# Optimization experiments

Hardware: AMD Instinct MI355X
Metric: run time of the kernel (lower is better)

The kernel has to match this reference:

```python
import jax, jax.numpy as jnp
import numpy as np
import math

DIM = 1024
HEADS = 16
DH = DIM // HEADS
HIDDEN = 4 * DIM
B, N = 2, 1024
DT = 0.05


def _cplx(r, i):
    return jax.lax.complex(r, i)


def clin(x, Wr, Wi, br, bi):
    # complex linear: (xr + i xi)(Wr + i Wi)^T + (br + i bi)
    xr, xi = x.real, x.imag
    real = xr @ Wr.T - xi @ Wi.T + br
    imag = xr @ Wi.T + xi @ Wr.T + bi
    return _cplx(real, imag)


def setup_inputs() -> dict:
    key = jax.random.key(0)
    ks = jax.random.split(key, 32)
    s = 0.02
    d = {
        'x_real': jax.random.normal(ks[0], (B, N, DIM), jnp.float32),
        'x_imag': jax.random.normal(ks[1], (B, N, DIM), jnp.float32),
    }
    i = 2
    for name in ['q', 'k', 'v', 'o']:
        d[f'Wr_{name}'] = jax.random.normal(ks[i], (DIM, DIM), jnp.float32) * s; i += 1
        d[f'Wi_{name}'] = jax.random.normal(ks[i], (DIM, DIM), jnp.float32) * s; i += 1
        d[f'br_{name}'] = jnp.zeros((DIM,), jnp.float32)
        d[f'bi_{name}'] = jnp.zeros((DIM,), jnp.float32)
    d['Wr_f1'] = jax.random.normal(ks[i], (HIDDEN, DIM), jnp.float32) * s; i += 1
    d['Wi_f1'] = jax.random.normal(ks[i], (HIDDEN, DIM), jnp.float32) * s; i += 1
    d['br_f1'] = jnp.zeros((HIDDEN,), jnp.float32)
    d['bi_f1'] = jnp.zeros((HIDDEN,), jnp.float32)
    d['Wr_f2'] = jax.random.normal(ks[i], (DIM, HIDDEN), jnp.float32) * s; i += 1
    d['Wi_f2'] = jax.random.normal(ks[i], (DIM, HIDDEN), jnp.float32) * s; i += 1
    d['br_f2'] = jnp.zeros((DIM,), jnp.float32)
    d['bi_f2'] = jnp.zeros((DIM,), jnp.float32)
    H0 = jax.random.normal(ks[i], (DIM, DIM), jnp.float32) * s; i += 1
    d['H'] = (H0 + H0.T) / 2
    d['dt'] = jnp.float32(DT)
    return d


def _forward(x_real, x_imag,
             Wr_q, Wi_q, br_q, bi_q, Wr_k, Wi_k, br_k, bi_k,
             Wr_v, Wi_v, br_v, bi_v, Wr_o, Wi_o, br_o, bi_o,
             Wr_f1, Wi_f1, br_f1, bi_f1, Wr_f2, Wi_f2, br_f2, bi_f2,
             H, dt):
    x = _cplx(x_real, x_imag)  # [B,N,D] complex64
    scale = 1.0 / math.sqrt(DH)

    # --- Quantum Fourier attention ---
    def heads(t):
        return t.reshape(B, N, HEADS, DH).transpose(0, 2, 1, 3)  # [B,H,N,dh]
    Q = heads(clin(x, Wr_q, Wi_q, br_q, bi_q))
    K = heads(clin(x, Wr_k, Wi_k, br_k, bi_k))
    V = heads(clin(x, Wr_v, Wi_v, br_v, bi_v))
    Qf = jnp.fft.fft(Q, axis=2)
    Kf = jnp.fft.fft(K, axis=2)
    Vf = jnp.fft.fft(V, axis=2)
    scores = jnp.einsum('bhid,bhjd->bhij', Qf, jnp.conj(Kf)) * scale
    attn = jax.nn.softmax(scores.real, axis=-1).astype(jnp.complex64)
    out_f = jnp.einsum('bhij,bhjd->bhid', attn, Vf)
    out = jnp.fft.ifft(out_f, axis=2).transpose(0, 2, 1, 3).reshape(B, N, DIM)
    attn_out = clin(out, Wr_o, Wi_o, br_o, bi_o)
    x = x + attn_out

    # --- Quantum feed-forward (GELU on real & imag separately, exact erf) ---
    h = clin(x, Wr_f1, Wi_f1, br_f1, bi_f1)
    h = _cplx(jax.nn.gelu(h.real, approximate=False),
              jax.nn.gelu(h.imag, approximate=False))
    x = x + clin(h, Wr_f2, Wi_f2, br_f2, bi_f2)

    # --- Schrodinger unitary evolution: U = expm(-i H dt) ---
    A = _cplx(jnp.zeros_like(H), -(H * dt))  # complex64
    U = jax.scipy.linalg.expm(A)
    out = (x.reshape(B * N, DIM) @ U).reshape(B, N, DIM)
    return out


def reference(x_real, x_imag,
              Wr_q, Wi_q, br_q, bi_q, Wr_k, Wi_k, br_k, bi_k,
              Wr_v, Wi_v, br_v, bi_v, Wr_o, Wi_o, br_o, bi_o,
              Wr_f1, Wi_f1, br_f1, bi_f1, Wr_f2, Wi_f2, br_f2, bi_f2,
              H, dt):
    out = _forward(x_real, x_imag,
                   Wr_q, Wi_q, br_q, bi_q, Wr_k, Wi_k, br_k, bi_k,
                   Wr_v, Wi_v, br_v, bi_v, Wr_o, Wi_o, br_o, bi_o,
                   Wr_f1, Wi_f1, br_f1, bi_f1, Wr_f2, Wi_f2, br_f2, bi_f2,
                   H, dt)
    # return real/imag stacked for easy real-valued comparison: [2,B,N,D]
    return jnp.stack([out.real, out.imag], axis=0)
```

## Files before the change

### kernel.cpp

```cpp
#include <hip/hip_runtime.h>
#include <cstdint>
#include <cstddef>

typedef unsigned int u32;
typedef unsigned short u16;
typedef long long i64;

typedef __attribute__((ext_vector_type(8))) short short8;
typedef __attribute__((ext_vector_type(4))) float f32x4;
typedef __attribute__((ext_vector_type(4))) int i32x4;

__device__ __forceinline__ u16 f2bf(float f) {
  u32 u = __float_as_uint(f);
  u = (u + 0x7FFFu + ((u >> 16) & 1u)) >> 16;
  return (u16)u;
}
__device__ __forceinline__ float bf2f(u16 h) { return __uint_as_float(((u32)h) << 16); }

__device__ __forceinline__ short8 neg8(short8 v) {
  i32x4 u = __builtin_bit_cast(i32x4, v);
  u = u ^ (int)0x80008000u;
  return __builtin_bit_cast(short8, u);
}
__device__ __forceinline__ f32x4 mfma16(short8 a, short8 b, f32x4 c) {
  return __builtin_amdgcn_mfma_f32_16x16x32_bf16(a, b, c, 0, 0, 0);
}
__device__ __forceinline__ float gelu_f(float x) {
  return 0.5f * x * (1.0f + erff(x * 0.7071067811865475f));
}
__device__ __forceinline__ void gl16(const u16* g, u16* l) {
  __builtin_amdgcn_global_load_lds((const __attribute__((address_space(1))) void*)g,
                                   (__attribute__((address_space(3))) void*)l, 16, 0, 0);
}
template <int N>
__device__ __forceinline__ void wait_barrier() {
  asm volatile("s_waitcnt vmcnt(%0)\n\ts_barrier" ::"i"(N) : "memory");
}

struct GemmP {
  const u16 *Arh, *Aih, *Arl, *Ail;
  const u16 *Brh, *Bih, *Brl, *Bil;
  const float *biasr, *biasi;
  const float *Resr, *Resi;
  float *Cr32, *Ci32;
  u16 *Crh, *Cih, *Crl, *Cil;
  i64 sA1, sA2, sB1, sB2, sC1, sC2;
  int ZH;
  int M, N, K, lda, ldb, ldc;
  float alpha;
  int beta, wb32, ctrans, bias_mode, bias_period, gelu, splitB;
  float bias_scale;
};

template <int CMODE, int SPLIT, int DEEP>
__global__ __launch_bounds__(256, 2) void cgemm_kernel(GemmP p) {
  constexpr bool HAS_CI = (CMODE == 0 || CMODE == 2 || CMODE == 3);
  constexpr bool AI = (CMODE == 0 || CMODE == 3);
  constexpr bool BIc = (CMODE == 0 || CMODE == 2 || CMODE == 3);
  constexpr int BUFU = SPLIT ? 24576 : 8192;
  constexpr int NBUF = DEEP ? 3 : 1;
  __shared__ u16 smem[BUFU * NBUF];
  constexpr int LPS64 = 2 + (AI ? 1 : 0) + (BIc ? 1 : 0);
  constexpr int NJ = SPLIT ? 4 : 2;

  const int tid = threadIdx.x, lane = tid & 63, wave = tid >> 6;
  const int lrow = lane & 15, quad = lane >> 4;
  const int wr = wave >> 1, wc = wave & 1;
  const int m0 = blockIdx.y * (SPLIT ? 128 : 64);
  const int n0 = blockIdx.x * 64;
  const int z1 = blockIdx.z / p.ZH, z2 = blockIdx.z % p.ZH;
  const i64 zA = (i64)z1 * p.sA1 + (i64)z2 * p.sA2;
  const i64 zB = (i64)z1 * p.sB1 + (i64)z2 * p.sB2;
  const i64 zC = (i64)z1 * p.sC1 + (i64)z2 * p.sC2;
  const int l4 = lane >> 2;
  const int lc = DEEP ? ((((lane & 3) ^ ((lane >> 3) & 3))) << 3) : ((lane & 3) << 3);
  const i64 aoff0 = zA + (i64)(m0 + (SPLIT ? 32 : 16) * wave + l4) * p.lda + lc;
  const i64 aoff1 = aoff0 + (i64)16 * p.lda;
  const i64 boff = zB + (i64)(n0 + 16 * wave + l4) * p.ldb + lc;
  const int lA0 = (SPLIT ? 1024 : 512) * wave, lA1 = lA0 + 512;
  const int lB0 = 512 * wave;
  const int cxw = ((lrow >> 1) & 3) << 3;

  f32x4 accR[2][NJ], accI[2][NJ];
  const f32x4 z4 = {0.f, 0.f, 0.f, 0.f};
#pragma unroll
  for (int i = 0; i < 2; ++i)
#pragma unroll
    for (int j = 0; j < NJ; ++j) { accR[i][j] = z4; accI[i][j] = z4; }

  const int ktn = p.K >> 5;

  if constexpr (SPLIT && !DEEP) {
    for (int kt = 0; kt < ktn; ++kt) {
      const i64 kc = (i64)(kt << 5);
      __syncthreads();
      gl16(p.Arh + aoff0 + kc, smem + lA0);
      gl16(p.Arh + aoff1 + kc, smem + lA1);
      gl16(p.Aih + aoff0 + kc, smem + 4096 + lA0);
      gl16(p.Aih + aoff1 + kc, smem + 4096 + lA1);
      gl16(p.Arl + aoff0 + kc, smem + 8192 + lA0);
      gl16(p.Arl + aoff1 + kc, smem + 8192 + lA1);
      gl16(p.Ail + aoff0 + kc, smem + 12288 + lA0);
      gl16(p.Ail + aoff1 + kc, smem + 12288 + lA1);
      gl16(p.Brh + boff + kc, smem + 16384 + lB0);
      gl16(p.Bih + boff + kc, smem + 18432 + lB0);
      if (p.splitB) {
        gl16(p.Brl + boff + kc, smem + 20480 + lB0);
        gl16(p.Bil + boff + kc, smem + 22528 + lB0);
      }
      __syncthreads();

      short8 bRh[4], bIh[4], bRl[4], bIl[4];
#pragma unroll
      for (int j = 0; j < 4; ++j) {
        const int off = (j * 16 + lrow) * 32 + quad * 8;
        bRh[j] = *(const short8*)&smem[16384 + off];
        bIh[j] = *(const short8*)&smem[18432 + off];
        if (p.splitB) {
          bRl[j] = *(const short8*)&smem[20480 + off];
          bIl[j] = *(const short8*)&smem[22528 + off];
        }
      }
#pragma unroll
      for (int i = 0; i < 2; ++i) {
        const int off = (wave * 32 + i * 16 + lrow) * 32 + quad * 8;
        short8 aRh = *(const short8*)&smem[off];
        short8 aIh = *(const short8*)&smem[4096 + off];
        short8 aRl = *(const short8*)&smem[8192 + off];
        short8 aIl = *(const short8*)&smem[12288 + off];
        if constexpr (CMODE == 0) {
          short8 nIh = neg8(aIh), nIl = neg8(aIl);
#pragma unroll
          for (int j = 0; j < 4; ++j) {
            accR[i][j] = mfma16(aRh, bRh[j], accR[i][j]);
            accR[i][j] = mfma16(nIh, bIh[j], accR[i][j]);
            accI[i][j] = mfma16(aRh, bIh[j], accI[i][j]);
            accI[i][j] = mfma16(aIh, bRh[j], accI[i][j]);
            accR[i][j] = mfma16(aRl, bRh[j], accR[i][j]);
            accR[i][j] = mfma16(nIl, bIh[j], accR[i][j]);
            accI[i][j] = mfma16(aRl, bIh[j], accI[i][j]);
            accI[i][j] = mfma16(aIl, bRh[j], accI[i][j]);
            if (p.splitB) {
              accR[i][j] = mfma16(aRh, bRl[j], accR[i][j]);
              accR[i][j] = mfma16(nIh, bIl[j], accR[i][j]);
              accI[i][j] = mfma16(aRh, bIl[j], accI[i][j]);
              accI[i][j] = mfma16(aIh, bRl[j], accI[i][j]);
            }
          }
        } else {
#pragma unroll
          for (int j = 0; j < 4; ++j) {
            accR[i][j] = mfma16(aRh, bRh[j], accR[i][j]);
            accR[i][j] = mfma16(aIh, bIh[j], accR[i][j]);
            accR[i][j] = mfma16(aRl, bRh[j], accR[i][j]);
            accR[i][j] = mfma16(aIl, bIh[j], accR[i][j]);
            accR[i][j] = mfma16(aRh, bRl[j], accR[i][j]);
            accR[i][j] = mfma16(aIh, bIl[j], accR[i][j]);
          }
        }
      }
    }
  } else if constexpr (SPLIT && DEEP) {
    auto stageS = [&](int buf, i64 kc) {
      u16* s = smem + buf * 24576;
      gl16(p.Arh + aoff0 + kc, s + lA0);
      gl16(p.Arh + aoff1 + kc, s + lA1);
      gl16(p.Aih + aoff0 + kc, s + 4096 + lA0);
      gl16(p.Aih + aoff1 + kc, s + 4096 + lA1);
      gl16(p.Arl + aoff0 + kc, s + 8192 + lA0);
      gl16(p.Arl + aoff1 + kc, s + 8192 + lA1);
      gl16(p.Ail + aoff0 + kc, s + 12288 + lA0);
      gl16(p.Ail + aoff1 + kc, s + 12288 + lA1);
      gl16(p.Brh + boff + kc, s + 16384 + lB0);
      gl16(p.Bih + boff + kc, s + 18432 + lB0);
      if (p.splitB) {
        gl16(p.Brl + boff + kc, s + 20480 + lB0);
        gl16(p.Bil + boff + kc, s + 22528 + lB0);
      }
    };
    if (ktn > 0) stageS(0, 0);
    if (ktn > 1) stageS(1, 32);
    for (int kt = 0; kt < ktn; ++kt) {
      if (kt + 1 < ktn) {
        if (p.splitB) wait_barrier<12>(); else wait_barrier<10>();
      } else {
        wait_barrier<0>();
      }
      if (kt + 2 < ktn) stageS((kt + 2) % 3, (i64)((kt + 2) << 5));
      const u16* sb = smem + (kt % 3) * 24576;

      short8 bRh[4], bIh[4], bRl[4], bIl[4];
#pragma unroll
      for (int j = 0; j < 4; ++j) {
        const int off = (j * 16 + lrow) * 32 + (quad * 8 ^ cxw);
        bRh[j] = *(const short8*)&sb[16384 + off];
        bIh[j] = *(const short8*)&sb[18432 + off];
        if (p.splitB) {
          bRl[j] = *(const short8*)&sb[20480 + off];
          bIl[j] = *(const short8*)&sb[22528 + off];
        }
      }
#pragma unroll
      for (int i = 0; i < 2; ++i) {
        const int off = (wave * 32 + i * 16 + lrow) * 32 + (quad * 8 ^ cxw);
        short8 aRh = *(const short8*)&sb[off];
        short8 aIh = *(const short8*)&sb[4096 + off];
        short8 aRl = *(const short8*)&sb[8192 + off];
        short8 aIl = *(const short8*)&sb[12288 + off];
        if constexpr (CMODE == 0) {
          short8 nIh = neg8(aIh), nIl = neg8(aIl);
#pragma unroll
          for (int j = 0; j < 4; ++j) {
            accR[i][j] = mfma16(aRh, bRh[j], accR[i][j]);
            accR[i][j] = mfma16(nIh, bIh[j], accR[i][j]);
            accI[i][j] = mfma16(aRh, bIh[j], accI[i][j]);
            accI[i][j] = mfma16(aIh, bRh[j], accI[i][j]);
            accR[i][j] = mfma16(aRl, bRh[j], accR[i][j]);
            accR[i][j] = mfma16(nIl, bIh[j], accR[i][j]);
            accI[i][j] = mfma16(aRl, bIh[j], accI[i][j]);
            accI[i][j] = mfma16(aIl, bRh[j], accI[i][j]);
            if (p.splitB) {
              accR[i][j] = mfma16(aRh, bRl[j], accR[i][j]);
              accR[i][j] = mfma16(nIh, bIl[j], accR[i][j]);
              accI[i][j] = mfma16(aRh, bIl[j], accI[i][j]);
              accI[i][j] = mfma16(aIh, bRl[j], accI[i][j]);
            }
          }
        } else {
#pragma unroll
          for (int j = 0; j < 4; ++j) {
            accR[i][j] = mfma16(aRh, bRh[j], accR[i][j]);
            accR[i][j] = mfma16(aIh, bIh[j], accR[i][j]);
            accR[i][j] = mfma16(aRl, bRh[j], accR[i][j]);
            accR[i][j] = mfma16(aIl, bIh[j], accR[i][j]);
            accR[i][j] = mfma16(aRh, bRl[j], accR[i][j]);
            accR[i][j] = mfma16(aIh, bIl[j], accR[i][j]);
          }
        }
      }
    }
  } else {
    auto stage = [&](int buf, i64 kc) {
      u16* s = smem + buf * 8192;
      gl16(p.Arh + aoff0 + kc, s + lA0);
      if constexpr (AI) gl16(p.Aih + aoff0 + kc, s + 2048 + lA0);
      gl16(p.Brh + boff + kc, s + 4096 + lB0);
      if constexpr (BIc) gl16(p.Bih + boff + kc, s + 6144 + lB0);
    };
    if (ktn > 0) stage(0, 0);
    if (ktn > 1) stage(1, 32);
    for (int kt = 0; kt < ktn; ++kt) {
      if (kt + 1 < ktn) wait_barrier<LPS64>(); else wait_barrier<0>();
      if (kt + 2 < ktn) stage((kt + 2) % 3, (i64)((kt + 2) << 5));
      const u16* sb = smem + (kt % 3) * 8192;

      short8 bR[2], bI[2];
#pragma unroll
      for (int j = 0; j < 2; ++j) {
        const int off = 4096 + (wc * 32 + j * 16 + lrow) * 32 + (quad * 8 ^ cxw);
        bR[j] = *(const short8*)&sb[off];
        if constexpr (BIc) bI[j] = *(const short8*)&sb[off + 2048];
      }
#pragma unroll
      for (int i = 0; i < 2; ++i) {
        const int off = (wr * 32 + i * 16 + lrow) * 32 + (quad * 8 ^ cxw);
        short8 aR = *(const short8*)&sb[off];
        if constexpr (CMODE == 0) {
          short8 aI = *(const short8*)&sb[off + 2048];
          short8 nI = neg8(aI);
#pragma unroll
          for (int j = 0; j < 2; ++j) {
            accR[i][j] = mfma16(aR, bR[j], accR[i][j]);
            accR[i][j] = mfma16(nI, bI[j], accR[i][j]);
            accI[i][j] = mfma16(aR, bI[j], accI[i][j]);
            accI[i][j] = mfma16(aI, bR[j], accI[i][j]);
          }
        } else if constexpr (CMODE == 1) {
#pragma unroll
          for (int j = 0; j < 2; ++j) accR[i][j] = mfma16(aR, bR[j], accR[i][j]);
        } else if constexpr (CMODE == 2) {
#pragma unroll
          for (int j = 0; j < 2; ++j) {
            accR[i][j] = mfma16(aR, bR[j], accR[i][j]);
            accI[i][j] = mfma16(aR, bI[j], accI[i][j]);
          }
        } else {
          short8 aI = *(const short8*)&sb[off + 2048];
          short8 nI = neg8(aI);
#pragma unroll
          for (int j = 0; j < 2; ++j) {
            accR[i][j] = mfma16(aR, bR[j], accR[i][j]);
            accR[i][j] = mfma16(aI, bI[j], accR[i][j]);
            accI[i][j] = mfma16(aR, bI[j], accI[i][j]);
            accI[i][j] = mfma16(nI, bR[j], accI[i][j]);
          }
        }
      }
    }
  }

#pragma unroll
  for (int i = 0; i < 2; ++i) {
#pragma unroll
    for (int j = 0; j < NJ; ++j) {
      const int gn = SPLIT ? (n0 + j * 16 + lrow) : (n0 + wc * 32 + j * 16 + lrow);
#pragma unroll
      for (int r = 0; r < 4; ++r) {
        const int gm = SPLIT ? (m0 + wave * 32 + i * 16 + quad * 4 + r)
                             : (m0 + wr * 32 + i * 16 + quad * 4 + r);
        const i64 idx = p.ctrans ? (zC + (i64)gn * p.ldc + gm) : (zC + (i64)gm * p.ldc + gn);
        float vr = accR[i][j][r] * p.alpha;
        float vi = 0.f;
        if (HAS_CI) vi = accI[i][j][r] * p.alpha;
        if (p.beta) {
          vr += p.Cr32[idx];
          if (HAS_CI && p.Ci32) vi += p.Ci32[idx];
        }
        if (p.bias_mode == 1) {
          vr += p.biasr[gn];
          if (HAS_CI) vi += p.biasi[gn];
        } else if (p.bias_mode == 2) {
          if ((gm % p.bias_period) == 0) {
            vr += p.biasr[gn] * p.bias_scale;
            if (HAS_CI) vi += p.biasi[gn] * p.bias_scale;
          }
        }
        if (p.Resr) vr += p.Resr[idx];
        if (HAS_CI && p.Resi) vi += p.Resi[idx];
        if (p.gelu) {
          vr = gelu_f(vr);
          if (HAS_CI) vi = gelu_f(vi);
        }
        if (p.wb32 && p.Cr32) p.Cr32[idx] = vr;
        if (p.wb32 && HAS_CI && p.Ci32) p.Ci32[idx] = vi;
        if (p.Crh) {
          const u16 hh = f2bf(vr);
          p.Crh[idx] = hh;
          if (p.Crl) p.Crl[idx] = f2bf(vr - bf2f(hh));
        }
        if (HAS_CI && p.Cih) {
          const u16 hh = f2bf(vi);
          p.Cih[idx] = hh;
          if (p.Cil) p.Cil[idx] = f2bf(vi - bf2f(hh));
        }
      }
    }
  }
}

struct CvtBatch {
  const float* src[12];
  u16* hi[12];
  u16* lo[12];
  i64 cum[13];
};
__global__ __launch_bounds__(256) void cvt_batch_kernel(CvtBatch b) {
  const i64 k = (i64)blockIdx.x * 1024 + (i64)threadIdx.x * 4;
  int s = 0;
  while (k >= b.cum[s + 1]) ++s;
  const i64 base = k - b.cum[s];
  float4 v = *(const float4*)(b.src[s] + base);
  u16* hp = b.hi[s];
  u16* lp = b.lo[s];
  ushort4 h, l;
  h.x = f2bf(v.x); l.x = f2bf(v.x - bf2f(h.x));
  h.y = f2bf(v.y); l.y = f2bf(v.y - bf2f(h.y));
  h.z = f2bf(v.z); l.z = f2bf(v.z - bf2f(h.z));
  h.w = f2bf(v.w); l.w = f2bf(v.w - bf2f(h.w));
  *(ushort4*)(hp + base) = h;
  if (lp) *(ushort4*)(lp + base) = l;
}

__global__ __launch_bounds__(256) void cvt_split_kernel(const float* in, u16* hi, u16* lo,
                                                        i64 n, const float* scale_ptr) {
  const i64 base = (i64)blockIdx.x * 1024 + (i64)threadIdx.x * 4;
  const float s = scale_ptr ? *scale_ptr : 1.0f;
#pragma unroll
  for (int e = 0; e < 4; ++e) {
    const i64 k = base + e;
    if (k < n) {
      const float v = in[k] * s;
      const u16 h = f2bf(v);
      hi[k] = h;
      if (lo) lo[k] = f2bf(v - bf2f(h));
    }
  }
}

__global__ __launch_bounds__(256) void trans_cvt_kernel(const float* in, u16* outh, u16* outl) {
  __shared__ float t[32][33];
  const int b = blockIdx.z;
  const int j0 = blockIdx.y * 32;
  const int d0 = blockIdx.x * 32;
  const int r = threadIdx.x >> 5, c = threadIdx.x & 31;
  const float* ip = in + (i64)b * 1048576;
#pragma unroll
  for (int it = 0; it < 4; ++it) t[r + it * 8][c] = ip[(i64)(j0 + r + it * 8) * 1024 + d0 + c];
  __syncthreads();
  u16* ohp = outh + (i64)b * 1048576;
  u16* olp = outl + (i64)b * 1048576;
#pragma unroll
  for (int it = 0; it < 4; ++it) {
    const float v = t[c][r + it * 8];
    const i64 o = (i64)(d0 + r + it * 8) * 1024 + j0 + c;
    const u16 h = f2bf(v);
    ohp[o] = h;
    olp[o] = f2bf(v - bf2f(h));
  }
}

__global__ __launch_bounds__(256) void gen_F_kernel(u16* Frh, u16* Frl, u16* Fih, u16* Fil) {
  const int idx = blockIdx.x * 256 + threadIdx.x;
  const int mm = idx >> 10, kk = idx & 1023;
  const int t = (mm * kk) & 1023;
  float sv, cv;
  sincosf((float)t * 6.135923151e-3f, &sv, &cv);
  const float fr = cv, fi = -sv;
  u16 h = f2bf(fr);
  Frh[idx] = h;
  Frl[idx] = f2bf(fr - bf2f(h));
  h = f2bf(fi);
  Fih[idx] = h;
  Fil[idx] = f2bf(fi - bf2f(h));
}

__global__ __launch_bounds__(256) void assemble_U_kernel(const float* X2m, const float* Hm,
                                                         const float* dtp, u16* Urh, u16* Uih) {
  const int idx = blockIdx.x * 256 + threadIdx.x;
  const int i = idx >> 10, j = idx & 1023;
  const float dt = *dtp;
  const float ur = ((i == j) ? 1.0f : 0.0f) - 0.5f * X2m[idx];
  const float ui = -dt * Hm[idx];
  Urh[idx] = f2bf(ur);
  Uih[idx] = f2bf(ui);
}

__global__ __launch_bounds__(256) void softmax_kernel(float* S) {
  float* row = S + (i64)blockIdx.x * 1024;
  const int t = threadIdx.x;
  float4 v = *(float4*)(row + t * 4);
  float m = fmaxf(fmaxf(v.x, v.y), fmaxf(v.z, v.w));
#pragma unroll
  for (int off = 32; off > 0; off >>= 1) m = fmaxf(m, __shfl_down(m, off));
  __shared__ float red[8];
  const int lane = t & 63, w = t >> 6;
  if (lane == 0) red[w] = m;
  __syncthreads();
  if (t == 0) red[4] = fmaxf(fmaxf(red[0], red[1]), fmaxf(red[2], red[3]));
  __syncthreads();
  m = red[4];
  v.x = expf(v.x - m);
  v.y = expf(v.y - m);
  v.z = expf(v.z - m);
  v.w = expf(v.w - m);
  float s = v.x + v.y + v.z + v.w;
#pragma unroll
  for (int off = 32; off > 0; off >>= 1) s += __shfl_down(s, off);
  if (lane == 0) red[w] = s;
  __syncthreads();
  if (t == 0) red[5] = red[0] + red[1] + red[2] + red[3];
  __syncthreads();
  const float inv = 1.0f / red[5];
  ushort4 o;
  o.x = f2bf(v.x * inv);
  o.y = f2bf(v.y * inv);
  o.z = f2bf(v.z * inv);
  o.w = f2bf(v.w * inv);
  *(ushort4*)((u16*)row + t * 4) = o;
}

static void run_gemm(hipStream_t s, int cmode, int split, int deep, const GemmP& p, int Z) {
  dim3 g((unsigned)(p.N >> 6), (unsigned)(p.M >> (split ? 7 : 6)), (unsigned)Z);
  dim3 b(256, 1, 1);
  if (split) {
    if (deep) hipLaunchKernelGGL(HIP_KERNEL_NAME(cgemm_kernel<0, 1, 1>), g, b, 0, s, p);
    else hipLaunchKernelGGL(HIP_KERNEL_NAME(cgemm_kernel<1, 1, 0>), g, b, 0, s, p);
  } else {
    if (cmode == 0) hipLaunchKernelGGL(HIP_KERNEL_NAME(cgemm_kernel<0, 0, 1>), g, b, 0, s, p);
    else if (cmode == 1) hipLaunchKernelGGL(HIP_KERNEL_NAME(cgemm_kernel<1, 0, 1>), g, b, 0, s, p);
    else if (cmode == 2) hipLaunchKernelGGL(HIP_KERNEL_NAME(cgemm_kernel<2, 0, 1>), g, b, 0, s, p);
    else hipLaunchKernelGGL(HIP_KERNEL_NAME(cgemm_kernel<3, 0, 1>), g, b, 0, s, p);
  }
}

extern "C" void kernel_launch(void* const* d_in, const int* in_sizes, int n_in, void* d_out,
                              int out_size, void* d_ws, size_t ws_size, hipStream_t stream) {
  (void)in_sizes; (void)n_in; (void)out_size; (void)ws_size;
  const float* x_real = (const float*)d_in[0];
  const float* x_imag = (const float*)d_in[1];
  const float* Wr_q = (const float*)d_in[2];
  const float* Wi_q = (const float*)d_in[3];
  const float* br_q = (const float*)d_in[4];
  const float* bi_q = (const float*)d_in[5];
  const float* Wr_k = (const float*)d_in[6];
  const float* Wi_k = (const float*)d_in[7];
  const float* br_k = (const float*)d_in[8];
  const float* bi_k = (const float*)d_in[9];
  const float* Wr_v = (const float*)d_in[10];
  const float* Wi_v = (const float*)d_in[11];
  const float* br_v = (const float*)d_in[12];
  const float* bi_v = (const float*)d_in[13];
  const float* Wr_o = (const float*)d_in[14];
  const float* Wi_o = (const float*)d_in[15];
  const float* br_o = (const float*)d_in[16];
  const float* bi_o = (const float*)d_in[17];
  const float* Wr_f1 = (const float*)d_in[18];
  const float* Wi_f1 = (const float*)d_in[19];
  const float* br_f1 = (const float*)d_in[20];
  const float* bi_f1 = (const float*)d_in[21];
  const float* Wr_f2 = (const float*)d_in[22];
  const float* Wi_f2 = (const float*)d_in[23];
  const float* br_f2 = (const float*)d_in[24];
  const float* bi_f2 = (const float*)d_in[25];
  const float* Hm = (const float*)d_in[26];
  const float* dtp = (const float*)d_in[27];

  const size_t MBy = 1ull << 20;
  char* W = (char*)d_ws;
  auto U16 = [&](size_t mb) { return (u16*)(W + mb * MBy); };
  auto F32p = [&](size_t mb) { return (float*)(W + mb * MBy); };

  float* scores = F32p(0);
  u16 *xT_rh = U16(0), *xT_ih = U16(4), *xT_rl = U16(8), *xT_il = U16(12);
  u16 *Wq_rh = U16(16), *Wq_ih = U16(18), *Wq_rl = U16(20), *Wq_il = U16(22);
  u16 *Wk_rh = U16(24), *Wk_ih = U16(26), *Wk_rl = U16(28), *Wk_il = U16(30);
  u16 *xf_rh = U16(32), *xf_ih = U16(36), *xf_rl = U16(40), *xf_il = U16(44);
  u16 *h_r = U16(64), *h_i = U16(80);
  u16 *x2_rh = U16(96), *x2_ih = U16(100), *x2_rl = U16(104), *x2_il = U16(108);
  u16* Xh = U16(112);
  float* X2m = F32p(114);
  u16 *Urh = U16(124), *Uih = U16(126);
  u16 *Wv_rh = U16(128), *Wv_ih = U16(130);
  u16 *Wo_rh = U16(132), *Wo_ih = U16(134);
  u16 *Wf1_rh = U16(136), *Wf1_ih = U16(144);
  u16 *Wf2_rh = U16(152), *Wf2_ih = U16(160);
  u16 *F_rh = U16(168), *F_ih = U16(170), *F_rl = U16(172), *F_il = U16(174);
  u16 *Qf_rh = U16(176), *Qf_ih = U16(180), *Qf_rl = U16(184), *Qf_il = U16(188);
  u16 *Kf_rh = U16(192), *Kf_ih = U16(196), *Kf_rl = U16(200), *Kf_il = U16(204);
  u16 *VfT_r = U16(208), *VfT_i = U16(212);
  u16 *ofT_r = U16(216), *ofT_i = U16(220);
  u16 *ot_r = U16(224), *ot_i = U16(228);
  float* x1_r = F32p(232);
  float* x1_i = F32p(240);
  u16 *x1h_r = U16(248), *x1h_i = U16(252);

  {
    CvtBatch b{};
    const float* srcs[12] = {Wr_q, Wi_q, Wr_k, Wi_k, Wr_v, Wi_v, Wr_o, Wi_o,
                             Wr_f1, Wi_f1, Wr_f2, Wi_f2};
    u16* his[12] = {Wq_rh, Wq_ih, Wk_rh, Wk_ih, Wv_rh, Wv_ih, Wo_rh, Wo_ih,
                    Wf1_rh, Wf1_ih, Wf2_rh, Wf2_ih};
    u16* los[12] = {Wq_rl, Wq_il, Wk_rl, Wk_il, nullptr, nullptr, nullptr, nullptr,
                    nullptr, nullptr, nullptr, nullptr};
    const i64 sizes[12] = {1048576, 1048576, 1048576, 1048576, 1048576, 1048576, 1048576,
                           1048576, 4194304, 4194304, 4194304, 4194304};
    i64 c = 0;
    for (int i = 0; i < 12; ++i) {
      b.src[i] = srcs[i]; b.hi[i] = his[i]; b.lo[i] = los[i];
      b.cum[i] = c; c += sizes[i];
    }
    b.cum[12] = c;
    hipLaunchKernelGGL(cvt_batch_kernel, dim3((unsigned)(c / 1024)), dim3(256), 0, stream, b);
  }
  hipLaunchKernelGGL(trans_cvt_kernel, dim3(32, 32, 2), dim3(256), 0, stream, x_real, xT_rh, xT_rl);
  hipLaunchKernelGGL(trans_cvt_kernel, dim3(32, 32, 2), dim3(256), 0, stream, x_imag, xT_ih, xT_il);
  hipLaunchKernelGGL(gen_F_kernel, dim3(4096), dim3(256), 0, stream, F_rh, F_rl, F_ih, F_il);

  GemmP p;
  auto clearp = [&]() {
    p = GemmP{};
    p.alpha = 1.0f;
    p.ZH = 1;
  };

  clearp();
  p.M = 1024; p.N = 1024; p.K = 1024; p.lda = 1024; p.ldb = 1024; p.ldc = 1024;
  p.sB1 = 1048576; p.sC1 = 1048576;
  p.Arh = F_rh; p.Aih = F_ih; p.Arl = F_rl; p.Ail = F_il;
  p.Brh = xT_rh; p.Bih = xT_ih; p.Brl = xT_rl; p.Bil = xT_il; p.splitB = 1;
  p.Crh = xf_rh; p.Cih = xf_ih; p.Crl = xf_rl; p.Cil = xf_il;
  run_gemm(stream, 0, 1, 1, p, 2);

  auto proj = [&](const u16* Wrh, const u16* Wih, const u16* Wrl, const u16* Wil,
                  const float* br, const float* bi, u16* Orh, u16* Oih, u16* Orl, u16* Oil) {
    clearp();
    p.M = 2048; p.N = 1024; p.K = 1024; p.lda = 1024; p.ldb = 1024; p.ldc = 1024;
    p.Arh = xf_rh; p.Aih = xf_ih; p.Arl = xf_rl; p.Ail = xf_il;
    p.Brh = Wrh; p.Bih = Wih; p.Brl = Wrl; p.Bil = Wil; p.splitB = 1;
    p.bias_mode = 2; p.bias_period = 1024; p.bias_scale = 1024.0f;
    p.biasr = br; p.biasi = bi;
    p.Crh = Orh; p.Cih = Oih; p.Crl = Orl; p.Cil = Oil;
    run_gemm(stream, 0, 1, 1, p, 1);
  };
  proj(Wq_rh, Wq_ih, Wq_rl, Wq_il, br_q, bi_q, Qf_rh, Qf_ih, Qf_rl, Qf_il);
  proj(Wk_rh, Wk_ih, Wk_rl, Wk_il, br_k, bi_k, Kf_rh, Kf_ih, Kf_rl, Kf_il);

  clearp();
  p.M = 1024; p.N = 1024; p.K = 1024; p.lda = 1024; p.ldb = 1024; p.ldc = 1024;
  p.sA1 = 1048576; p.sC1 = 1048576;
  p.Arh = xf_rh; p.Aih = xf_ih; p.Brh = Wv_rh; p.Bih = Wv_ih;
  p.bias_mode = 2; p.bias_period = 1024; p.bias_scale = 1024.0f;
  p.biasr = br_v; p.biasi = bi_v;
  p.ctrans = 1;
  p.Crh = VfT_r; p.Cih = VfT_i;
  run_gemm(stream, 0, 0, 1, p, 2);

  clearp();
  p.M = 1024; p.N = 1024; p.K = 64; p.lda = 1024; p.ldb = 1024; p.ldc = 1024;
  p.ZH = 16;
  p.sA1 = 1048576; p.sA2 = 64; p.sB1 = 1048576; p.sB2 = 64;
  p.sC1 = 16ll * 1048576; p.sC2 = 1048576;
  p.alpha = 0.125f;
  p.Arh = Qf_rh; p.Aih = Qf_ih; p.Arl = Qf_rl; p.Ail = Qf_il;
  p.Brh = Kf_rh; p.Bih = Kf_ih; p.Brl = Kf_rl; p.Bil = Kf_il; p.splitB = 1;
  p.Cr32 = scores; p.wb32 = 1;
  run_gemm(stream, 1, 1, 0, p, 32);

  hipLaunchKernelGGL(softmax_kernel, dim3(32768), dim3(256), 0, stream, scores);

  clearp();
  p.M = 1024; p.N = 64; p.K = 1024; p.lda = 2048; p.ldb = 1024; p.ldc = 1024;
  p.ZH = 16;
  p.sA1 = 16ll * 2097152; p.sA2 = 2097152;
  p.sB1 = 1048576; p.sB2 = 65536;
  p.sC1 = 1048576; p.sC2 = 65536;
  p.ctrans = 1;
  p.Arh = (const u16*)scores; p.Brh = VfT_r; p.Bih = VfT_i;
  p.Crh = ofT_r; p.Cih = ofT_i;
  run_gemm(stream, 2, 0, 1, p, 32);

  clearp();
  p.M = 1024; p.N = 1024; p.K = 1024; p.lda = 1024; p.ldb = 1024; p.ldc = 1024;
  p.sB1 = 1048576; p.sC1 = 1048576;
  p.alpha = 1.0f / 1024.0f;
  p.Arh = F_rh; p.Aih = F_ih; p.Brh = ofT_r; p.Bih = ofT_i;
  p.Crh = ot_r; p.Cih = ot_i;
  run_gemm(stream, 3, 0, 1, p, 2);

  clearp();
  p.M = 2048; p.N = 1024; p.K = 1024; p.lda = 1024; p.ldb = 1024; p.ldc = 1024;
  p.Arh = ot_r; p.Aih = ot_i; p.Brh = Wo_rh; p.Bih = Wo_ih;
  p.bias_mode = 1; p.biasr = br_o; p.biasi = bi_o;
  p.Resr = x_real; p.Resi = x_imag;
  p.Cr32 = x1_r; p.Ci32 = x1_i; p.wb32 = 1; p.Crh = x1h_r; p.Cih = x1h_i;
  run_gemm(stream, 0, 0, 1, p, 1);

  clearp();
  p.M = 2048; p.N = 4096; p.K = 1024; p.lda = 1024; p.ldb = 1024; p.ldc = 4096;
  p.Arh = x1h_r; p.Aih = x1h_i; p.Brh = Wf1_rh; p.Bih = Wf1_ih;
  p.bias_mode = 1; p.biasr = br_f1; p.biasi = bi_f1;
  p.gelu = 1;
  p.Crh = h_r; p.Cih = h_i;
  run_gemm(stream, 0, 0, 1, p, 1);

  clearp();
  p.M = 2048; p.N = 1024; p.K = 4096; p.lda = 4096; p.ldb = 4096; p.ldc = 1024;
  p.Arh = h_r; p.Aih = h_i; p.Brh = Wf2_rh; p.Bih = Wf2_ih;
  p.bias_mode = 1; p.biasr = br_f2; p.biasi = bi_f2;
  p.Resr = x1_r; p.Resi = x1_i;
  p.Crh = x2_rh; p.Cih = x2_ih; p.Crl = x2_rl; p.Cil = x2_il;
  run_gemm(stream, 0, 0, 1, p, 1);

  hipLaunchKernelGGL(cvt_split_kernel, dim3(1024), dim3(256), 0, stream, Hm, Xh,
                     (u16*)nullptr, (i64)1048576, dtp);

  clearp();
  p.M = 1024; p.N = 1024; p.K = 1024; p.lda = 1024; p.ldb = 1024; p.ldc = 1024;
  p.Arh = Xh; p.Brh = Xh;
  p.Cr32 = X2m; p.wb32 = 1;
  run_gemm(stream, 1, 0, 1, p, 1);
  hipLaunchKernelGGL(assemble_U_kernel, dim3(4096), dim3(256), 0, stream, X2m, Hm, dtp, Urh, Uih);

  float* out_r = (float*)d_out;
  float* out_i = out_r + 2097152;
  clearp();
  p.M = 2048; p.N = 1024; p.K = 1024; p.lda = 1024; p.ldb = 1024; p.ldc = 1024;
  p.Arh = x2_rh; p.Aih = x2_ih; p.Arl = x2_rl; p.Ail = x2_il;
  p.Brh = Urh; p.Bih = Uih; p.splitB = 0;
  p.Cr32 = out_r; p.Ci32 = out_i; p.wb32 = 1;
  run_gemm(stream, 0, 1, 1, p, 1);
}
```

Before: 909.4 us.

## Shrink split-precision complex GEMM tile to 64x64 with 2x2 wave layout

The deep-pipelined split-bf16 complex GEMM path moves from a 128x64 block tile, where each wave owns 32 rows, to a 64x64 tile with a 2x2 wave grid. It also makes the B low-part split a compile-time variant (DEEP==2: no B lo, triple buffer; DEEP==1: B lo, double buffer). This launches twice as many blocks and uses less LDS per block, aiming at better occupancy and CU coverage for the final 2048x1024x1024 product with U. The cost is less operand reuse per block and more global and LDS traffic per FLOP.

```diff
diff --git a/kernel.cpp b/kernel.cpp
--- a/kernel.cpp
+++ b/kernel.cpp
@@ -57,16 +57,18 @@
   constexpr bool HAS_CI = (CMODE == 0 || CMODE == 2 || CMODE == 3);
   constexpr bool AI = (CMODE == 0 || CMODE == 3);
   constexpr bool BIc = (CMODE == 0 || CMODE == 2 || CMODE == 3);
-  constexpr int BUFU = SPLIT ? 24576 : 8192;
-  constexpr int NBUF = DEEP ? 3 : 1;
+  constexpr bool OLD128 = (SPLIT && DEEP == 0);
+  constexpr int SB = (DEEP == 2) ? 2 : 4;
+  constexpr int BUFU = SPLIT ? (DEEP == 0 ? 24576 : (DEEP == 2 ? 12288 : 16384)) : 8192;
+  constexpr int NBUF = DEEP ? ((SPLIT && DEEP == 1) ? 2 : 3) : 1;
   __shared__ u16 smem[BUFU * NBUF];
   constexpr int LPS64 = 2 + (AI ? 1 : 0) + (BIc ? 1 : 0);
-  constexpr int NJ = SPLIT ? 4 : 2;
+  constexpr int NJ = OLD128 ? 4 : 2;
 
   const int tid = threadIdx.x, lane = tid & 63, wave = tid >> 6;
   const int lrow = lane & 15, quad = lane >> 4;
   const int wr = wave >> 1, wc = wave & 1;
-  const int m0 = blockIdx.y * (SPLIT ? 128 : 64);
+  const int m0 = blockIdx.y * (OLD128 ? 128 : 64);
   const int n0 = blockIdx.x * 64;
   const int z1 = blockIdx.z / p.ZH, z2 = blockIdx.z % p.ZH;
   const i64 zA = (i64)z1 * p.sA1 + (i64)z2 * p.sA2;
@@ -74,10 +76,10 @@
   const i64 zC = (i64)z1 * p.sC1 + (i64)z2 * p.sC2;
   const int l4 = lane >> 2;
   const int lc = DEEP ? ((((lane & 3) ^ ((lane >> 3) & 3))) << 3) : ((lane & 3) << 3);
-  const i64 aoff0 = zA + (i64)(m0 + (SPLIT ? 32 : 16) * wave + l4) * p.lda + lc;
+  const i64 aoff0 = zA + (i64)(m0 + (OLD128 ? 32 : 16) * wave + l4) * p.lda + lc;
   const i64 aoff1 = aoff0 + (i64)16 * p.lda;
   const i64 boff = zB + (i64)(n0 + 16 * wave + l4) * p.ldb + lc;
-  const int lA0 = (SPLIT ? 1024 : 512) * wave, lA1 = lA0 + 512;
+  const int lA0 = (OLD128 ? 1024 : 512) * wave, lA1 = lA0 + 512;
   const int lB0 = 512 * wave;
   const int cxw = ((lrow >> 1) & 3) << 3;
 
@@ -90,7 +92,7 @@
 
   const int ktn = p.K >> 5;
 
-  if constexpr (SPLIT && !DEEP) {
+  if constexpr (SPLIT && DEEP == 0) {
     for (int kt = 0; kt < ktn; ++kt) {
       const i64 kc = (i64)(kt << 5);
       __syncthreads();
@@ -160,81 +162,66 @@
         }
       }
     }
-  } else if constexpr (SPLIT && DEEP) {
+  } else if constexpr (SPLIT && DEEP >= 1) {
     auto stageS = [&](int buf, i64 kc) {
-      u16* s = smem + buf * 24576;
+      u16* s = smem + buf * BUFU;
       gl16(p.Arh + aoff0 + kc, s + lA0);
-      gl16(p.Arh + aoff1 + kc, s + lA1);
-      gl16(p.Aih + aoff0 + kc, s + 4096 + lA0);
-      gl16(p.Aih + aoff1 + kc, s + 4096 + lA1);
-      gl16(p.Arl + aoff0 + kc, s + 8192 + lA0);
-      gl16(p.Arl + aoff1 + kc, s + 8192 + lA1);
-      gl16(p.Ail + aoff0 + kc, s + 12288 + lA0);
-      gl16(p.Ail + aoff1 + kc, s + 12288 + lA1);
-      gl16(p.Brh + boff + kc, s + 16384 + lB0);
-      gl16(p.Bih + boff + kc, s + 18432 + lB0);
-      if (p.splitB) {
-        gl16(p.Brl + boff + kc, s + 20480 + lB0);
-        gl16(p.Bil + boff + kc, s + 22528 + lB0);
+      gl16(p.Aih + aoff0 + kc, s + 2048 + lA0);
+      gl16(p.Arl + aoff0 + kc, s + 4096 + lA0);
+      gl16(p.Ail + aoff0 + kc, s + 6144 + lA0);
+      gl16(p.Brh + boff + kc, s + 8192 + lB0);
+      gl16(p.Bih + boff + kc, s + 10240 + lB0);
+      if constexpr (SB == 4) {
+        gl16(p.Brl + boff + kc, s + 12288 + lB0);
+        gl16(p.Bil + boff + kc, s + 14336 + lB0);
       }
     };
     if (ktn > 0) stageS(0, 0);
-    if (ktn > 1) stageS(1, 32);
+    if (DEEP == 2 && ktn > 1) stageS(1, 32);
     for (int kt = 0; kt < ktn; ++kt) {
-      if (kt + 1 < ktn) {
-        if (p.splitB) wait_barrier<12>(); else wait_barrier<10>();
+      if constexpr (DEEP == 1) {
+        wait_barrier<0>();
+        if (kt + 1 < ktn) stageS((kt + 1) & 1, (i64)((kt + 1) << 5));
       } else {
-        wait_barrier<0>();
-      }
-      if (kt + 2 < ktn) stageS((kt + 2) % 3, (i64)((kt + 2) << 5));
-      const u16* sb = smem + (kt % 3) * 24576;
-
-      short8 bRh[4], bIh[4], bRl[4], bIl[4];
-#pragma unroll
-      for (int j = 0; j < 4; ++j) {
-        const int off = (j * 16 + lrow) * 32 + (quad * 8 ^ cxw);
-        bRh[j] = *(const short8*)&sb[16384 + off];
-        bIh[j] = *(const short8*)&sb[18432 + off];
-        if (p.splitB) {
-          bRl[j] = *(const short8*)&sb[20480 + off];
-          bIl[j] = *(const short8*)&sb[22528 + off];
+        if (kt + 1 < ktn) wait_barrier<6>(); else wait_barrier<0>();
+        if (kt + 2 < ktn) stageS((kt + 2) % 3, (i64)((kt + 2) << 5));
+      }
+      const u16* sb = smem + (DEEP == 1 ? (kt & 1) : (kt % 3)) * BUFU;
+
+      short8 bRh[2], bIh[2], bRl[2], bIl[2];
+#pragma unroll
+      for (int j = 0; j < 2; ++j) {
+        const int off = 8192 + (wc * 32 + j * 16 + lrow) * 32 + (quad * 8 ^ cxw);
+        bRh[j] = *(const short8*)&sb[off];
+        bIh[j] = *(const short8*)&sb[off + 2048];
+        if constexpr (SB == 4) {
+          bRl[j] = *(const short8*)&sb[off + 4096];
+          bIl[j] = *(const short8*)&sb[off + 6144];
         }
       }
 #pragma unroll
       for (int i = 0; i < 2; ++i) {
-        const int off = (wave * 32 + i * 16 + lrow) * 32 + (quad * 8 ^ cxw);
+        const int off = (wr * 32 + i * 16 + lrow) * 32 + (quad * 8 ^ cxw);
         short8 aRh = *(const short8*)&sb[off];
-        short8 aIh = *(const short8*)&sb[4096 + off];
-        short8 aRl = *(const short8*)&sb[8192 + off];
-        short8 aIl = *(const short8*)&sb[12288 + off];
-        if constexpr (CMODE == 0) {
-          short8 nIh = neg8(aIh), nIl = neg8(aIl);
-#pragma unroll
-          for (int j = 0; j < 4; ++j) {
-            accR[i][j] = mfma16(aRh, bRh[j], accR[i][j]);
-            accR[i][j] = mfma16(nIh, bIh[j], accR[i][j]);
-            accI[i][j] = mfma16(aRh, bIh[j], accI[i][j]);
-            accI[i][j] = mfma16(aIh, bRh[j], accI[i][j]);
-            accR[i][j] = mfma16(aRl, bRh[j], accR[i][j]);
-            accR[i][j] = mfma16(nIl, bIh[j], accR[i][j]);
-            accI[i][j] = mfma16(aRl, bIh[j], accI[i][j]);
-            accI[i][j] = mfma16(aIl, bRh[j], accI[i][j]);
-            if (p.splitB) {
-              accR[i][j] = mfma16(aRh, bRl[j], accR[i][j]);
-              accR[i][j] = mfma16(nIh, bIl[j], accR[i][j]);
-              accI[i][j] = mfma16(aRh, bIl[j], accI[i][j]);
-              accI[i][j] = mfma16(aIh, bRl[j], accI[i][j]);
-            }
-          }
-        } else {
-#pragma unroll
-          for (int j = 0; j < 4; ++j) {
-            accR[i][j] = mfma16(aRh, bRh[j], accR[i][j]);
-            accR[i][j] = mfma16(aIh, bIh[j], accR[i][j]);
-            accR[i][j] = mfma16(aRl, bRh[j], accR[i][j]);
-            accR[i][j] = mfma16(aIl, bIh[j], accR[i][j]);
+        short8 aIh = *(const short8*)&sb[off + 2048];
+        short8 aRl = *(const short8*)&sb[off + 4096];
+        short8 aIl = *(const short8*)&sb[off + 6144];
+        short8 nIh = neg8(aIh), nIl = neg8(aIl);
+#pragma unroll
+        for (int j = 0; j < 2; ++j) {
+          accR[i][j] = mfma16(aRh, bRh[j], accR[i][j]);
+          accR[i][j] = mfma16(nIh, bIh[j], accR[i][j]);
+          accI[i][j] = mfma16(aRh, bIh[j], accI[i][j]);
+          accI[i][j] = mfma16(aIh, bRh[j], accI[i][j]);
+          accR[i][j] = mfma16(aRl, bRh[j], accR[i][j]);
+          accR[i][j] = mfma16(nIl, bIh[j], accR[i][j]);
+          accI[i][j] = mfma16(aRl, bIh[j], accI[i][j]);
+          accI[i][j] = mfma16(aIl, bRh[j], accI[i][j]);
+          if constexpr (SB == 4) {
             accR[i][j] = mfma16(aRh, bRl[j], accR[i][j]);
-            accR[i][j] = mfma16(aIh, bIl[j], accR[i][j]);
+            accR[i][j] = mfma16(nIh, bIl[j], accR[i][j]);
+            accI[i][j] = mfma16(aRh, bIl[j], accI[i][j]);
+            accI[i][j] = mfma16(aIh, bRl[j], accI[i][j]);
           }
         }
       }
@@ -303,11 +290,11 @@
   for (int i = 0; i < 2; ++i) {
 #pragma unroll
     for (int j = 0; j < NJ; ++j) {
-      const int gn = SPLIT ? (n0 + j * 16 + lrow) : (n0 + wc * 32 + j * 16 + lrow);
+      const int gn = OLD128 ? (n0 + j * 16 + lrow) : (n0 + wc * 32 + j * 16 + lrow);
 #pragma unroll
       for (int r = 0; r < 4; ++r) {
-        const int gm = SPLIT ? (m0 + wave * 32 + i * 16 + quad * 4 + r)
-                             : (m0 + wr * 32 + i * 16 + quad * 4 + r);
+        const int gm = OLD128 ? (m0 + wave * 32 + i * 16 + quad * 4 + r)
+                              : (m0 + wr * 32 + i * 16 + quad * 4 + r);
         const i64 idx = p.ctrans ? (zC + (i64)gn * p.ldc + gm) : (zC + (i64)gm * p.ldc + gn);
         float vr = accR[i][j][r] * p.alpha;
         float vi = 0.f;
@@ -470,10 +457,12 @@
 }
 
 static void run_gemm(hipStream_t s, int cmode, int split, int deep, const GemmP& p, int Z) {
-  dim3 g((unsigned)(p.N >> 6), (unsigned)(p.M >> (split ? 7 : 6)), (unsigned)Z);
+  const int mshift = (split && deep == 0) ? 7 : 6;
+  dim3 g((unsigned)(p.N >> 6), (unsigned)(p.M >> mshift), (unsigned)Z);
   dim3 b(256, 1, 1);
   if (split) {
-    if (deep) hipLaunchKernelGGL(HIP_KERNEL_NAME(cgemm_kernel<0, 1, 1>), g, b, 0, s, p);
+    if (deep == 1) hipLaunchKernelGGL(HIP_KERNEL_NAME(cgemm_kernel<0, 1, 1>), g, b, 0, s, p);
+    else if (deep == 2) hipLaunchKernelGGL(HIP_KERNEL_NAME(cgemm_kernel<0, 1, 2>), g, b, 0, s, p);
     else hipLaunchKernelGGL(HIP_KERNEL_NAME(cgemm_kernel<1, 1, 0>), g, b, 0, s, p);
   } else {
     if (cmode == 0) hipLaunchKernelGGL(HIP_KERNEL_NAME(cgemm_kernel<0, 0, 1>), g, b, 0, s, p);
@@ -678,5 +667,5 @@
   p.Arh = x2_rh; p.Aih = x2_ih; p.Arl = x2_rl; p.Ail = x2_il;
   p.Brh = Urh; p.Bih = Uih; p.splitB = 0;
   p.Cr32 = out_r; p.Ci32 = out_i; p.wb32 = 1;
-  run_gemm(stream, 0, 1, 1, p, 1);
-}
+  run_gemm(stream, 0, 1, 2, p, 1);
+}
```

After: 858.7 us. -5.6%, faster.
